# Kernel optimization log

Measured on AMD Instinct MI355X. Metric: run time of the kernel, lower is better.

## Reference

```python
import jax, jax.numpy as jnp
import numpy as np


def setup_inputs() -> dict:
    key = jax.random.key(0)
    distance = jax.random.uniform(key, (16, 2048, 1024), dtype=jnp.float32)
    return {"distance": distance}


def reference(distance):
    # distance: (..., data_length, max_distance)
    original_shape = distance.shape
    L, M = original_shape[-2], original_shape[-1]
    d = distance.reshape(-1, L, M)  # (B, L, M)
    r = jnp.arange(M, dtype=d.dtype)  # range over max_distance

    # weighted mean distance per batch element
    col_sum = d.sum(axis=-2)                                   # (B, M)
    mean_distance = (col_sum * r).sum(axis=-1) / col_sum.sum(axis=-1)  # (B,)
    scales = mean_distance / (0.5 * M)                         # (B,)

    # data-dependent resampling indices along the max_distance axis
    new_idx = (scales[:, None] * r[None, :]).astype(jnp.int32)  # (B, M)
    # TF clips to max_distance (inclusive); gather then reads index M-1 under
    # JAX's clip semantics, which matches clipping to M-1 here.
    new_idx = jnp.clip(new_idx, 0, M - 1)

    idx = jnp.broadcast_to(new_idx[:, None, :], d.shape)        # (B, L, M)
    normed = jnp.take_along_axis(d, idx, axis=-1)               # (B, L, M)
    return normed.reshape(original_shape)
```

## Files before the change

### kernel.cpp

```cpp
#include <hip/hip_runtime.h>


constexpr int L = 2048;
constexpr int M = 1024;
constexpr int LCH = 64;
constexpr int ROWS = L / LCH;

__global__ __launch_bounds__(256) void colsum_partial(
    const float* __restrict__ d, float* __restrict__ partial) {
    const int blk = blockIdx.x;
    const int b   = blk / LCH;
    const int lch = blk % LCH;
    const int t   = threadIdx.x;

    const float* base = d + ((size_t)b * L + (size_t)lch * ROWS) * M + t * 4;
    float4 acc = make_float4(0.f, 0.f, 0.f, 0.f);
#pragma unroll 4
    for (int l = 0; l < ROWS; ++l) {
        float4 v = *reinterpret_cast<const float4*>(base + (size_t)l * M);
        acc.x += v.x; acc.y += v.y; acc.z += v.z; acc.w += v.w;
    }
    *reinterpret_cast<float4*>(partial + ((size_t)b * LCH + lch) * M + t * 4) = acc;
}

__global__ __launch_bounds__(256) void scale_and_idx(
    const float* __restrict__ partial, int* __restrict__ new_idx) {
    const int b = blockIdx.x;
    const int t = threadIdx.x;
    const int m0 = t * 4;

    double c0 = 0.0, c1 = 0.0, c2 = 0.0, c3 = 0.0;
    for (int lch = 0; lch < LCH; ++lch) {
        float4 v = *reinterpret_cast<const float4*>(
            partial + ((size_t)b * LCH + lch) * M + m0);
        c0 += v.x; c1 += v.y; c2 += v.z; c3 += v.w;
    }
    double s0 = c0 + c1 + c2 + c3;
    double s1 = c0 * (double)m0 + c1 * (double)(m0 + 1) +
                c2 * (double)(m0 + 2) + c3 * (double)(m0 + 3);

#pragma unroll
    for (int off = 32; off > 0; off >>= 1) {
        s0 += __shfl_down(s0, off);
        s1 += __shfl_down(s1, off);
    }
    __shared__ double ls0[4], ls1[4];
    const int wave = t >> 6, lane = t & 63;
    if (lane == 0) { ls0[wave] = s0; ls1[wave] = s1; }
    __syncthreads();
    __shared__ float sscale;
    if (t == 0) {
        double S0 = ls0[0] + ls0[1] + ls0[2] + ls0[3];
        double S1 = ls1[0] + ls1[1] + ls1[2] + ls1[3];
        double mean = S1 / S0;
        sscale = (float)(mean / (0.5 * (double)M));
    }
    __syncthreads();
    const float sc = sscale;

    int4 o;
    o.x = min(max((int)(sc * (float)(m0 + 0)), 0), M - 1);
    o.y = min(max((int)(sc * (float)(m0 + 1)), 0), M - 1);
    o.z = min(max((int)(sc * (float)(m0 + 2)), 0), M - 1);
    o.w = min(max((int)(sc * (float)(m0 + 3)), 0), M - 1);
    *reinterpret_cast<int4*>(new_idx + (size_t)b * M + m0) = o;
}

__global__ __launch_bounds__(256) void gather_rows(
    const float* __restrict__ d, const int* __restrict__ new_idx,
    float* __restrict__ out) {
    const int blk = blockIdx.x;
    const int b   = blk >> 11;
    const int t   = threadIdx.x;

    const float* row = d + (size_t)blk * M;
    const int4 idx = *reinterpret_cast<const int4*>(new_idx + (size_t)b * M + t * 4);
    float4 v;
    v.x = row[idx.x];
    v.y = row[idx.y];
    v.z = row[idx.z];
    v.w = row[idx.w];
    *reinterpret_cast<float4*>(out + (size_t)blk * M + t * 4) = v;
}

extern "C" void kernel_launch(void* const* d_in, const int* in_sizes, int n_in,
                              void* d_out, int out_size, void* d_ws, size_t ws_size,
                              hipStream_t stream) {
    const float* d = (const float*)d_in[0];
    float* out = (float*)d_out;
    const int n = in_sizes[0];
    const int B = n / (L * M);

    float* partial = (float*)d_ws;
    int* new_idx   = (int*)((char*)d_ws + (size_t)B * LCH * M * sizeof(float));

    colsum_partial<<<B * LCH, 256, 0, stream>>>(d, partial);
    scale_and_idx<<<B, 256, 0, stream>>>(partial, new_idx);
    gather_rows<<<B * L, 256, 0, stream>>>(d, new_idx, out);
}
```

Measured before the change: 260.8 us.

## Fuse scale computation into colsum and gather, process multiple rows per block

The partial column-sum kernel now reduces each chunk fully to two double sums (weighted and unweighted), which removes the per-batch partial buffer and the separate scale_and_idx kernel. The gather kernel combines the 64 chunk sums, computes the scale and indices itself, then processes eight rows per block with nontemporal stores. This cuts one launch, a workspace round trip and per-row index loads. In exchange, every gather block redundantly recomputes the scale, and the colsum blocks do more reduction work.

New measurement: 248.1 us. 1.05x faster.

```diff
diff --git a/kernel.cpp b/kernel.cpp
--- a/kernel.cpp
+++ b/kernel.cpp
@@ -1,43 +1,33 @@
 #include <hip/hip_runtime.h>
 
 
-constexpr int L = 2048;
-constexpr int M = 1024;
-constexpr int LCH = 64;
+typedef float f32x4 __attribute__((ext_vector_type(4)));
+
+constexpr int L    = 2048;
+constexpr int M    = 1024;
+constexpr int LCH  = 64;
 constexpr int ROWS = L / LCH;
+constexpr int RPB  = 8;
+constexpr int GPB  = L / RPB;
 
-__global__ __launch_bounds__(256) void colsum_partial(
-    const float* __restrict__ d, float* __restrict__ partial) {
+__global__ __launch_bounds__(256) void colsum_reduce(
+    const float* __restrict__ d, double* __restrict__ sums) {
     const int blk = blockIdx.x;
     const int b   = blk / LCH;
     const int lch = blk % LCH;
     const int t   = threadIdx.x;
+    const int m0  = t * 4;
 
-    const float* base = d + ((size_t)b * L + (size_t)lch * ROWS) * M + t * 4;
-    float4 acc = make_float4(0.f, 0.f, 0.f, 0.f);
-#pragma unroll 4
+    const float* base = d + ((size_t)b * L + (size_t)lch * ROWS) * M + m0;
+    float a0 = 0.f, a1 = 0.f, a2 = 0.f, a3 = 0.f;
+#pragma unroll 8
     for (int l = 0; l < ROWS; ++l) {
-        float4 v = *reinterpret_cast<const float4*>(base + (size_t)l * M);
-        acc.x += v.x; acc.y += v.y; acc.z += v.z; acc.w += v.w;
+        f32x4 v = *reinterpret_cast<const f32x4*>(base + (size_t)l * M);
+        a0 += v.x; a1 += v.y; a2 += v.z; a3 += v.w;
     }
-    *reinterpret_cast<float4*>(partial + ((size_t)b * LCH + lch) * M + t * 4) = acc;
-}
-
-__global__ __launch_bounds__(256) void scale_and_idx(
-    const float* __restrict__ partial, int* __restrict__ new_idx) {
-    const int b = blockIdx.x;
-    const int t = threadIdx.x;
-    const int m0 = t * 4;
-
-    double c0 = 0.0, c1 = 0.0, c2 = 0.0, c3 = 0.0;
-    for (int lch = 0; lch < LCH; ++lch) {
-        float4 v = *reinterpret_cast<const float4*>(
-            partial + ((size_t)b * LCH + lch) * M + m0);
-        c0 += v.x; c1 += v.y; c2 += v.z; c3 += v.w;
-    }
-    double s0 = c0 + c1 + c2 + c3;
-    double s1 = c0 * (double)m0 + c1 * (double)(m0 + 1) +
-                c2 * (double)(m0 + 2) + c3 * (double)(m0 + 3);
+    double s0 = (double)a0 + (double)a1 + (double)a2 + (double)a3;
+    double s1 = (double)a0 * (double)(m0 + 0) + (double)a1 * (double)(m0 + 1) +
+                (double)a2 * (double)(m0 + 2) + (double)a3 * (double)(m0 + 3);
 
 #pragma unroll
     for (int off = 32; off > 0; off >>= 1) {
@@ -48,39 +38,55 @@
     const int wave = t >> 6, lane = t & 63;
     if (lane == 0) { ls0[wave] = s0; ls1[wave] = s1; }
     __syncthreads();
-    __shared__ float sscale;
     if (t == 0) {
         double S0 = ls0[0] + ls0[1] + ls0[2] + ls0[3];
         double S1 = ls1[0] + ls1[1] + ls1[2] + ls1[3];
-        double mean = S1 / S0;
-        sscale = (float)(mean / (0.5 * (double)M));
+        sums[2 * (size_t)blk + 0] = S0;
+        sums[2 * (size_t)blk + 1] = S1;
+    }
+}
+
+__global__ __launch_bounds__(256) void gather_rows(
+    const float* __restrict__ d, const double* __restrict__ sums,
+    float* __restrict__ out) {
+    const int blk = blockIdx.x;
+    const int b   = blk / GPB;
+    const int l0  = (blk % GPB) * RPB;
+    const int t   = threadIdx.x;
+
+    __shared__ float sscale;
+    if (t < 64) {
+        double s0 = sums[(size_t)b * (2 * LCH) + 2 * t + 0];
+        double s1 = sums[(size_t)b * (2 * LCH) + 2 * t + 1];
+#pragma unroll
+        for (int off = 32; off > 0; off >>= 1) {
+            s0 += __shfl_down(s0, off);
+            s1 += __shfl_down(s1, off);
+        }
+        if (t == 0) sscale = (float)((s1 / s0) / (0.5 * (double)M));
     }
     __syncthreads();
     const float sc = sscale;
 
-    int4 o;
-    o.x = min(max((int)(sc * (float)(m0 + 0)), 0), M - 1);
-    o.y = min(max((int)(sc * (float)(m0 + 1)), 0), M - 1);
-    o.z = min(max((int)(sc * (float)(m0 + 2)), 0), M - 1);
-    o.w = min(max((int)(sc * (float)(m0 + 3)), 0), M - 1);
-    *reinterpret_cast<int4*>(new_idx + (size_t)b * M + m0) = o;
-}
+    const int m0 = t * 4;
+    const int i0 = min(max((int)(sc * (float)(m0 + 0)), 0), M - 1);
+    const int i1 = min(max((int)(sc * (float)(m0 + 1)), 0), M - 1);
+    const int i2 = min(max((int)(sc * (float)(m0 + 2)), 0), M - 1);
+    const int i3 = min(max((int)(sc * (float)(m0 + 3)), 0), M - 1);
 
-__global__ __launch_bounds__(256) void gather_rows(
-    const float* __restrict__ d, const int* __restrict__ new_idx,
-    float* __restrict__ out) {
-    const int blk = blockIdx.x;
-    const int b   = blk >> 11;
-    const int t   = threadIdx.x;
-
-    const float* row = d + (size_t)blk * M;
-    const int4 idx = *reinterpret_cast<const int4*>(new_idx + (size_t)b * M + t * 4);
-    float4 v;
-    v.x = row[idx.x];
-    v.y = row[idx.y];
-    v.z = row[idx.z];
-    v.w = row[idx.w];
-    *reinterpret_cast<float4*>(out + (size_t)blk * M + t * 4) = v;
+    const float* rowbase = d   + ((size_t)b * L + l0) * M;
+    float*       outbase = out + ((size_t)b * L + l0) * M;
+#pragma unroll
+    for (int r = 0; r < RPB; ++r) {
+        const float* row = rowbase + (size_t)r * M;
+        f32x4 v;
+        v.x = row[i0];
+        v.y = row[i1];
+        v.z = row[i2];
+        v.w = row[i3];
+        __builtin_nontemporal_store(v,
+            reinterpret_cast<f32x4*>(outbase + (size_t)r * M + m0));
+    }
 }
 
 extern "C" void kernel_launch(void* const* d_in, const int* in_sizes, int n_in,
@@ -91,10 +97,8 @@
     const int n = in_sizes[0];
     const int B = n / (L * M);
 
-    float* partial = (float*)d_ws;
-    int* new_idx   = (int*)((char*)d_ws + (size_t)B * LCH * M * sizeof(float));
+    double* sums = (double*)d_ws;
 
-    colsum_partial<<<B * LCH, 256, 0, stream>>>(d, partial);
-    scale_and_idx<<<B, 256, 0, stream>>>(partial, new_idx);
-    gather_rows<<<B * L, 256, 0, stream>>>(d, new_idx, out);
+    colsum_reduce<<<B * LCH, 256, 0, stream>>>(d, sums);
+    gather_rows<<<B * GPB, 256, 0, stream>>>(d, sums, out);
 }
```
